# Kernel optimization log

Measured on AMD Instinct MI355X. Metric: run time of the kernel, lower is better.

## Reference

```python
import jax, jax.numpy as jnp
import numpy as np

DIM = 1024
H = 16
DH = 64
INTER = H * DH

def setup_inputs() -> dict:
    key = jax.random.key(0)
    k1, k2, k3, k4 = jax.random.split(key, 4)
    input = jax.random.normal(k1, (4, 2048, DIM), dtype=jnp.float32)
    # nn.Linear weights stored as [out, in]; we keep [in, out] for x @ W
    W_qkv = jax.random.normal(k2, (DIM, INTER * 3), dtype=jnp.float32) * 0.02
    W_mlp = jax.random.normal(k3, (INTER, DIM), dtype=jnp.float32) * 0.02
    b_mlp = jax.random.normal(k4, (DIM,), dtype=jnp.float32) * 0.02
    return {"input": input, "W_qkv": W_qkv, "W_mlp": W_mlp, "b_mlp": b_mlp}

def reference(input, W_qkv, W_mlp, b_mlp):
    b, n, _ = input.shape
    qkv = input @ W_qkv                      # [b, n, 3*h*d]
    qkv = qkv.reshape(b, n, 3, H, DH)        # matches '(qkv h d)' split order
    qkv = jnp.transpose(qkv, (2, 0, 3, 1, 4))  # [3, b, h, n, d]
    q, k, v = qkv[0], qkv[1], qkv[2]
    scale = DH ** -0.5
    attn = jnp.einsum('bhnd,bhmd->bhnm', q, k) * scale
    attn = jax.nn.softmax(attn, axis=-1)
    out = jnp.einsum('bhnm,bhmd->bhnd', attn, v)
    out = jnp.transpose(out, (0, 2, 1, 3)).reshape(b, n, INTER)  # 'b h n d -> b n (h d)'
    return out @ W_mlp + b_mlp
```

## Files before the change

kernel.cpp:

```cpp
#include <hip/hip_runtime.h>
#include <stdint.h>

typedef __attribute__((ext_vector_type(8))) short bf16x8;
typedef __attribute__((ext_vector_type(4))) float f32x4;
typedef __attribute__((ext_vector_type(16))) float f32x16;

#define MFMA16(a, b, c) __builtin_amdgcn_mfma_f32_16x16x32_bf16((a), (b), (c), 0, 0, 0)
#define MFMA32(a, b, c) __builtin_amdgcn_mfma_f32_32x32x16_bf16((a), (b), (c), 0, 0, 0)

__device__ __forceinline__ unsigned short f2bf(float x) {
  uint32_t u = __float_as_uint(x);
  u += 0x7fffu + ((u >> 16) & 1u);
  return (unsigned short)(u >> 16);
}

__device__ __forceinline__ uint32_t cvt_pk_bf16(float a, float b) {
  uint32_t r;
  asm("v_cvt_pk_bf16_f32 %0, %1, %2" : "=v"(r) : "v"(a), "v"(b));
  return r;
}

__device__ __forceinline__ float exp2_hw(float x) {
  float r;
  asm("v_exp_f32 %0, %1" : "=v"(r) : "v"(x));
  return r;
}

__device__ __forceinline__ void gload_lds16(const void* g, void* l) {
  __builtin_amdgcn_global_load_lds(
      (const __attribute__((address_space(1))) uint32_t*)g,
      (__attribute__((address_space(3))) uint32_t*)l, 16, 0, 0);
}

__global__ __launch_bounds__(256) void prep_kernel(
    const float* __restrict__ X, unsigned short* __restrict__ Xb,
    const float* __restrict__ Wq, unsigned short* __restrict__ Wqt,
    const float* __restrict__ Wm, unsigned short* __restrict__ Wmt) {
  __shared__ float tile[64][65];
  const int bid = blockIdx.x;
  const int t = threadIdx.x;
  if (bid < 4096) {
    const int i = bid * 256 + t;
    const float4 a = *(const float4*)(X + (size_t)i * 8);
    const float4 b = *(const float4*)(X + (size_t)i * 8 + 4);
    uint4 o;
    o.x = (uint32_t)f2bf(a.x) | ((uint32_t)f2bf(a.y) << 16);
    o.y = (uint32_t)f2bf(a.z) | ((uint32_t)f2bf(a.w) << 16);
    o.z = (uint32_t)f2bf(b.x) | ((uint32_t)f2bf(b.y) << 16);
    o.w = (uint32_t)f2bf(b.z) | ((uint32_t)f2bf(b.w) << 16);
    *(uint4*)(Xb + (size_t)i * 8) = o;
    return;
  }
  const float* src;
  unsigned short* dst;
  int Nd, lb;
  if (bid < 4864) { src = Wq; dst = Wqt; Nd = 3072; lb = bid - 4096; }
  else            { src = Wm; dst = Wmt; Nd = 1024; lb = bid - 4864; }
  const int Kd = 1024;
  const int ntc = Nd >> 6;
  const int r0 = (lb / ntc) << 6;
  const int c0 = (lb % ntc) << 6;
  const int tr = t >> 4;
  const int tc4 = (t & 15) << 2;
#pragma unroll
  for (int p = 0; p < 4; ++p) {
    int row = p * 16 + tr;
    float4 v = *(const float4*)(src + (size_t)(r0 + row) * Nd + c0 + tc4);
    tile[row][tc4 + 0] = v.x;
    tile[row][tc4 + 1] = v.y;
    tile[row][tc4 + 2] = v.z;
    tile[row][tc4 + 3] = v.w;
  }
  __syncthreads();
#pragma unroll
  for (int p = 0; p < 4; ++p) {
    int c = p * 16 + tr;
    int r4 = (t & 15) << 2;
    uint2 pv;
    pv.x = (uint32_t)f2bf(tile[r4 + 0][c]) | ((uint32_t)f2bf(tile[r4 + 1][c]) << 16);
    pv.y = (uint32_t)f2bf(tile[r4 + 2][c]) | ((uint32_t)f2bf(tile[r4 + 3][c]) << 16);
    *(uint2*)(dst + (size_t)(c0 + c) * Kd + r0 + r4) = pv;
  }
}

__global__ __launch_bounds__(256) void gemm_qkv_kernel(
    const unsigned short* __restrict__ A,
    const unsigned short* __restrict__ Bt,
    unsigned short* __restrict__ Qo,
    unsigned short* __restrict__ Ko,
    unsigned short* __restrict__ Vo) {
  constexpr int Kdim = 1024, BK = 64;
  __shared__ unsigned short lA[128 * BK];
  __shared__ unsigned short lB[128 * BK];
  const int nbn = 24;
  const int wg = (blockIdx.x & 7) * 192 + (blockIdx.x >> 3);
  const int bi = wg / nbn, bj = wg % nbn;
  const int tid = threadIdx.x;
  const int l = tid & 63, w = tid >> 6;
  const int wr = w >> 1, wc = w & 1;
  const int lr = l & 15, lg = l >> 4;

  const f32x4 vzero = {0.f, 0.f, 0.f, 0.f};
  f32x4 acc[4][4];
#pragma unroll
  for (int i = 0; i < 4; ++i)
#pragma unroll
    for (int j = 0; j < 4; ++j) acc[i][j] = vzero;

  const int srow = tid >> 3;
  const int sc = tid & 7;
  const int sg = sc ^ (srow & 7);
  const unsigned short* As = A + (size_t)(bi * 128 + srow) * Kdim + sg * 8;
  const unsigned short* Bs = Bt + (size_t)(bj * 128 + srow) * Kdim + sg * 8;
  unsigned short* dA = &lA[(srow * 8 + sc) * 8];
  unsigned short* dB = &lB[(srow * 8 + sc) * 8];

  for (int kt = 0; kt < Kdim / BK; ++kt) {
    const int k0 = kt * BK;
#pragma unroll
    for (int rr = 0; rr < 4; ++rr) {
      gload_lds16(As + (size_t)rr * 32 * Kdim + k0, dA + rr * 32 * BK);
      gload_lds16(Bs + (size_t)rr * 32 * Kdim + k0, dB + rr * 32 * BK);
    }
    __syncthreads();
#pragma unroll
    for (int kk = 0; kk < 2; ++kk) {
      bf16x8 af[4], bfr[4];
#pragma unroll
      for (int it = 0; it < 4; ++it) {
        int r = wr * 64 + it * 16 + lr;
        af[it] = *(const bf16x8*)&lA[r * BK + (((kk * 4 + lg) ^ (lr & 7)) * 8)];
      }
#pragma unroll
      for (int jt = 0; jt < 4; ++jt) {
        int r = wc * 64 + jt * 16 + lr;
        bfr[jt] = *(const bf16x8*)&lB[r * BK + (((kk * 4 + lg) ^ (lr & 7)) * 8)];
      }
#pragma unroll
      for (int it = 0; it < 4; ++it)
#pragma unroll
        for (int jt = 0; jt < 4; ++jt)
          acc[it][jt] = MFMA16(af[it], bfr[jt], acc[it][jt]);
    }
    __syncthreads();
  }

#pragma unroll
  for (int jt = 0; jt < 4; ++jt) {
    const int col = bj * 128 + wc * 64 + jt * 16 + lr;
    const int s = col >> 10;
    const int rem = col & 1023;
    const int h = rem >> 6, d = rem & 63;
#pragma unroll
    for (int it = 0; it < 4; ++it) {
      const int m0 = bi * 128 + wr * 64 + it * 16 + lg * 4;
      const int b = m0 >> 11, n = m0 & 2047;
      const size_t bh = (size_t)b * 16 + h;
      if (s == 2) {
        uint2 pv;
        pv.x = (uint32_t)f2bf(acc[it][jt][0]) | ((uint32_t)f2bf(acc[it][jt][1]) << 16);
        pv.y = (uint32_t)f2bf(acc[it][jt][2]) | ((uint32_t)f2bf(acc[it][jt][3]) << 16);
        *(uint2*)(Vo + ((bh * 256 + (n >> 3)) * 64 + d) * 8 + (n & 7)) = pv;
      } else if (s == 1) {
        const size_t base = ((bh * 8 + (d >> 3)) * 2048) * 8 + (d & 7);
#pragma unroll
        for (int rg = 0; rg < 4; ++rg)
          Ko[base + (size_t)(n + rg) * 8] = f2bf(acc[it][jt][rg]);
      } else {
#pragma unroll
        for (int rg = 0; rg < 4; ++rg)
          Qo[(bh * 2048 + (size_t)(n + rg)) * 64 + d] = f2bf(acc[it][jt][rg] * 0.18033688011112042f);
      }
    }
  }
}

template <int T>
__device__ __forceinline__ bf16x8 build_pa(const f32x16& s, int hi) {
  uint32_t A1 = cvt_pk_bf16(s[T * 8 + 0], s[T * 8 + 1]);
  uint32_t A2 = cvt_pk_bf16(s[T * 8 + 2], s[T * 8 + 3]);
  uint32_t B1 = cvt_pk_bf16(s[T * 8 + 4], s[T * 8 + 5]);
  uint32_t B2 = cvt_pk_bf16(s[T * 8 + 6], s[T * 8 + 7]);
  uint32_t send1 = hi ? A1 : B1;
  uint32_t send2 = hi ? A2 : B2;
  uint32_t recv1 = (uint32_t)__shfl_xor((int)send1, 32);
  uint32_t recv2 = (uint32_t)__shfl_xor((int)send2, 32);
  union { uint32_t u[4]; bf16x8 v; } r;
  r.u[0] = hi ? recv1 : A1;
  r.u[1] = hi ? recv2 : A2;
  r.u[2] = hi ? B1 : recv1;
  r.u[3] = hi ? B2 : recv2;
  return r.v;
}

__device__ __forceinline__ float tile_sum(const f32x16& a, const f32x16& b) {
  float st[8];
#pragma unroll
  for (int i = 0; i < 8; ++i) st[i] = (a[i] + a[i + 8]) + (b[i] + b[i + 8]);
  float sm = ((st[0] + st[1]) + (st[2] + st[3])) + ((st[4] + st[5]) + (st[6] + st[7]));
  sm += __shfl_xor(sm, 32);
  return sm;
}

#define STAGE(NB, T)                                                              \
  {                                                                               \
    const int kv0_ = (T) * 64;                                                    \
    gload_lds16(KgB + (size_t)(0 * 2048 + kv0_) * 8 + (size_t)(w) * 2048 * 8,     \
                &lK[NB][w][l][0]);                                                \
    gload_lds16(KgB + (size_t)(4 * 2048 + kv0_) * 8 + (size_t)(w) * 2048 * 8,     \
                &lK[NB][w + 4][l][0]);                                            \
    gload_lds16(VgB + (size_t)(((T) * 8 + w) * 64) * 8, &lV[NB][w][l][0]);        \
    gload_lds16(VgB + (size_t)(((T) * 8 + w + 4) * 64) * 8, &lV[NB][w + 4][l][0]);\
  }

__global__ __launch_bounds__(256, 2) void attn_kernel(
    const unsigned short* __restrict__ Qg,
    const unsigned short* __restrict__ Kg,
    const unsigned short* __restrict__ Vg,
    unsigned short* __restrict__ AO) {
  __shared__ unsigned short lK[2][8][64][8];
  __shared__ unsigned short lV[2][8][64][8];
  const int bid = blockIdx.x;
  const int bh = (bid & 7) * 8 + (bid >> 6);
  const int qt = (bid >> 3) & 7;
  const int tid = threadIdx.x;
  const int l = tid & 63, w = tid >> 6;
  const int lo = l & 31, hi = l >> 5;
  const int qb = qt * 256 + w * 64;

  bf16x8 qfA[4], qfB[4];
  {
    const unsigned short* qrowA = Qg + ((size_t)bh * 2048 + qb + lo) * 64 + hi * 8;
    const unsigned short* qrowB = qrowA + 32 * 64;
#pragma unroll
    for (int ds = 0; ds < 4; ++ds) {
      qfA[ds] = *(const bf16x8*)(qrowA + ds * 16);
      qfB[ds] = *(const bf16x8*)(qrowB + ds * 16);
    }
  }

  f32x16 oA0, oA1, oB0, oB1;
#pragma unroll
  for (int i = 0; i < 16; ++i) { oA0[i] = 0.f; oA1[i] = 0.f; oB0[i] = 0.f; oB1[i] = 0.f; }
  float lA_ = 0.f, lB_ = 0.f;

  const unsigned short* KgB = Kg + (size_t)bh * 8 * 2048 * 8 + (size_t)l * 8;
  const unsigned short* VgB = Vg + (size_t)bh * 256 * 64 * 8 + (size_t)l * 8;

  STAGE(0, 0);
  int buf = 0;
  for (int t = 0; t < 32; ++t) {
    if (t < 31) {
      STAGE(buf ^ 1, t + 1);
      asm volatile("s_waitcnt vmcnt(8)" ::: "memory");
    } else {
      asm volatile("s_waitcnt vmcnt(0)" ::: "memory");
    }
    __builtin_amdgcn_s_barrier();
    __builtin_amdgcn_sched_barrier(0);

    f32x16 sA0, sA1, sB0, sB1;
#pragma unroll
    for (int i = 0; i < 16; ++i) { sA0[i] = 0.f; sA1[i] = 0.f; sB0[i] = 0.f; sB1[i] = 0.f; }
    __builtin_amdgcn_s_setprio(1);
#pragma unroll
    for (int ds = 0; ds < 4; ++ds) {
      bf16x8 k0 = *(const bf16x8*)&lK[buf][2 * ds + hi][lo][0];
      bf16x8 k1 = *(const bf16x8*)&lK[buf][2 * ds + hi][lo + 32][0];
      sA0 = MFMA32(k0, qfA[ds], sA0);
      sA1 = MFMA32(k1, qfA[ds], sA1);
      sB0 = MFMA32(k0, qfB[ds], sB0);
      sB1 = MFMA32(k1, qfB[ds], sB1);
    }
    __builtin_amdgcn_s_setprio(0);

#pragma unroll
    for (int i = 0; i < 16; ++i) { sA0[i] = exp2_hw(sA0[i]); sA1[i] = exp2_hw(sA1[i]); }
#pragma unroll
    for (int i = 0; i < 16; ++i) { sB0[i] = exp2_hw(sB0[i]); sB1[i] = exp2_hw(sB1[i]); }
    lA_ += tile_sum(sA0, sA1);
    lB_ += tile_sum(sB0, sB1);

    bf16x8 paA[4] = {build_pa<0>(sA0, hi), build_pa<1>(sA0, hi),
                     build_pa<0>(sA1, hi), build_pa<1>(sA1, hi)};
    bf16x8 paB[4] = {build_pa<0>(sB0, hi), build_pa<1>(sB0, hi),
                     build_pa<0>(sB1, hi), build_pa<1>(sB1, hi)};

    __builtin_amdgcn_s_setprio(1);
#pragma unroll
    for (int ks = 0; ks < 4; ++ks) {
      bf16x8 v0 = *(const bf16x8*)&lV[buf][2 * ks + hi][lo][0];
      bf16x8 v1 = *(const bf16x8*)&lV[buf][2 * ks + hi][lo + 32][0];
      oA0 = MFMA32(v0, paA[ks], oA0);
      oA1 = MFMA32(v1, paA[ks], oA1);
      oB0 = MFMA32(v0, paB[ks], oB0);
      oB1 = MFMA32(v1, paB[ks], oB1);
    }
    __builtin_amdgcn_s_setprio(0);
    __builtin_amdgcn_sched_barrier(0);
    __builtin_amdgcn_s_barrier();
    buf ^= 1;
  }

  const float linvA = 1.0f / lA_;
  const float linvB = 1.0f / lB_;
  const int b = bh >> 4, h = bh & 15;
  unsigned short* dstA = AO + ((size_t)(b * 2048 + qb + lo) * 1024 + h * 64 + 4 * hi);
  unsigned short* dstB = dstA + (size_t)32 * 1024;
#pragma unroll
  for (int q4 = 0; q4 < 4; ++q4) {
    uint2 p0;
    p0.x = cvt_pk_bf16(oA0[q4 * 4 + 0] * linvA, oA0[q4 * 4 + 1] * linvA);
    p0.y = cvt_pk_bf16(oA0[q4 * 4 + 2] * linvA, oA0[q4 * 4 + 3] * linvA);
    *(uint2*)(dstA + q4 * 8) = p0;
    uint2 p1;
    p1.x = cvt_pk_bf16(oA1[q4 * 4 + 0] * linvA, oA1[q4 * 4 + 1] * linvA);
    p1.y = cvt_pk_bf16(oA1[q4 * 4 + 2] * linvA, oA1[q4 * 4 + 3] * linvA);
    *(uint2*)(dstA + 32 + q4 * 8) = p1;
    uint2 p2;
    p2.x = cvt_pk_bf16(oB0[q4 * 4 + 0] * linvB, oB0[q4 * 4 + 1] * linvB);
    p2.y = cvt_pk_bf16(oB0[q4 * 4 + 2] * linvB, oB0[q4 * 4 + 3] * linvB);
    *(uint2*)(dstB + q4 * 8) = p2;
    uint2 p3;
    p3.x = cvt_pk_bf16(oB1[q4 * 4 + 0] * linvB, oB1[q4 * 4 + 1] * linvB);
    p3.y = cvt_pk_bf16(oB1[q4 * 4 + 2] * linvB, oB1[q4 * 4 + 3] * linvB);
    *(uint2*)(dstB + 32 + q4 * 8) = p3;
  }
}

__global__ __launch_bounds__(256) void gemm_mlp_kernel(
    const unsigned short* __restrict__ A,
    const unsigned short* __restrict__ Bt,
    const float* __restrict__ bias,
    float* __restrict__ out) {
  constexpr int Kdim = 1024, BK = 64;
  __shared__ unsigned short lA[128 * BK];
  __shared__ unsigned short lB[128 * BK];
  const int nbn = 8;
  const int wg = (blockIdx.x & 7) * 64 + (blockIdx.x >> 3);
  const int bi = wg / nbn, bj = wg % nbn;
  const int tid = threadIdx.x;
  const int l = tid & 63, w = tid >> 6;
  const int wr = w >> 1, wc = w & 1;
  const int lr = l & 15, lg = l >> 4;

  const f32x4 vzero = {0.f, 0.f, 0.f, 0.f};
  f32x4 acc[4][4];
#pragma unroll
  for (int i = 0; i < 4; ++i)
#pragma unroll
    for (int j = 0; j < 4; ++j) acc[i][j] = vzero;

  const int srow = tid >> 3;
  const int sc = tid & 7;
  const int sg = sc ^ (srow & 7);
  const unsigned short* As = A + (size_t)(bi * 128 + srow) * Kdim + sg * 8;
  const unsigned short* Bs = Bt + (size_t)(bj * 128 + srow) * Kdim + sg * 8;
  unsigned short* dA = &lA[(srow * 8 + sc) * 8];
  unsigned short* dB = &lB[(srow * 8 + sc) * 8];

  for (int kt = 0; kt < Kdim / BK; ++kt) {
    const int k0 = kt * BK;
#pragma unroll
    for (int rr = 0; rr < 4; ++rr) {
      gload_lds16(As + (size_t)rr * 32 * Kdim + k0, dA + rr * 32 * BK);
      gload_lds16(Bs + (size_t)rr * 32 * Kdim + k0, dB + rr * 32 * BK);
    }
    __syncthreads();
#pragma unroll
    for (int kk = 0; kk < 2; ++kk) {
      bf16x8 af[4], bfr[4];
#pragma unroll
      for (int it = 0; it < 4; ++it) {
        int r = wr * 64 + it * 16 + lr;
        af[it] = *(const bf16x8*)&lA[r * BK + (((kk * 4 + lg) ^ (lr & 7)) * 8)];
      }
#pragma unroll
      for (int jt = 0; jt < 4; ++jt) {
        int r = wc * 64 + jt * 16 + lr;
        bfr[jt] = *(const bf16x8*)&lB[r * BK + (((kk * 4 + lg) ^ (lr & 7)) * 8)];
      }
#pragma unroll
      for (int it = 0; it < 4; ++it)
#pragma unroll
        for (int jt = 0; jt < 4; ++jt)
          acc[it][jt] = MFMA16(af[it], bfr[jt], acc[it][jt]);
    }
    __syncthreads();
  }

#pragma unroll
  for (int jt = 0; jt < 4; ++jt) {
    const int col = bj * 128 + wc * 64 + jt * 16 + lr;
    const float bv = bias[col];
#pragma unroll
    for (int it = 0; it < 4; ++it) {
      const int m0 = bi * 128 + wr * 64 + it * 16 + lg * 4;
#pragma unroll
      for (int rg = 0; rg < 4; ++rg)
        out[(size_t)(m0 + rg) * 1024 + col] = acc[it][jt][rg] + bv;
    }
  }
}

extern "C" void kernel_launch(void* const* d_in, const int* in_sizes, int n_in,
                              void* d_out, int out_size, void* d_ws, size_t ws_size,
                              hipStream_t stream) {
  const float* X = (const float*)d_in[0];
  const float* Wqkv = (const float*)d_in[1];
  const float* Wmlp = (const float*)d_in[2];
  const float* bmlp = (const float*)d_in[3];
  float* out = (float*)d_out;

  char* ws = (char*)d_ws;
  unsigned short* Xb  = (unsigned short*)(ws);
  unsigned short* Wqt = (unsigned short*)(ws + 16777216);
  unsigned short* Wmt = (unsigned short*)(ws + 23068672);
  unsigned short* Qb  = (unsigned short*)(ws + 25165824);
  unsigned short* Kb  = (unsigned short*)(ws + 41943040);
  unsigned short* Vb  = (unsigned short*)(ws + 58720256);
  unsigned short* AOb = (unsigned short*)(ws + 75497472);

  prep_kernel<<<5120, 256, 0, stream>>>(X, Xb, Wqkv, Wqt, Wmlp, Wmt);
  gemm_qkv_kernel<<<1536, 256, 0, stream>>>(Xb, Wqt, Qb, Kb, Vb);
  attn_kernel<<<512, 256, 0, stream>>>(Qb, Kb, Vb, AOb);
  gemm_mlp_kernel<<<512, 256, 0, stream>>>(AOb, Wmt, bmlp, out);
}
```

Measured before the change: 192.8 us.

## Load K/V fragments directly from global into registers, dropping LDS staging

Replaces the double-buffered LDS staging of K and V tiles, with its block barriers, by direct per-wave global loads into registers. K for the next tile is prefetched after the QK MFMAs, and V is loaded at the top of each iteration. This removes the LDS traffic and the two barriers per iteration, but each of the four waves now fetches the same K/V data from global/L2 separately. It also raises register pressure and gives less latency hiding for the V loads.

```diff
diff --git a/kernel.cpp b/kernel.cpp
--- a/kernel.cpp
+++ b/kernel.cpp
@@ -202,24 +202,11 @@
   return sm;
 }
 
-#define STAGE(NB, T)                                                              \
-  {                                                                               \
-    const int kv0_ = (T) * 64;                                                    \
-    gload_lds16(KgB + (size_t)(0 * 2048 + kv0_) * 8 + (size_t)(w) * 2048 * 8,     \
-                &lK[NB][w][l][0]);                                                \
-    gload_lds16(KgB + (size_t)(4 * 2048 + kv0_) * 8 + (size_t)(w) * 2048 * 8,     \
-                &lK[NB][w + 4][l][0]);                                            \
-    gload_lds16(VgB + (size_t)(((T) * 8 + w) * 64) * 8, &lV[NB][w][l][0]);        \
-    gload_lds16(VgB + (size_t)(((T) * 8 + w + 4) * 64) * 8, &lV[NB][w + 4][l][0]);\
-  }
-
 __global__ __launch_bounds__(256, 2) void attn_kernel(
     const unsigned short* __restrict__ Qg,
     const unsigned short* __restrict__ Kg,
     const unsigned short* __restrict__ Vg,
     unsigned short* __restrict__ AO) {
-  __shared__ unsigned short lK[2][8][64][8];
-  __shared__ unsigned short lV[2][8][64][8];
   const int bid = blockIdx.x;
   const int bh = (bid & 7) * 8 + (bid >> 6);
   const int qt = (bid >> 3) & 7;
@@ -244,20 +231,22 @@
   for (int i = 0; i < 16; ++i) { oA0[i] = 0.f; oA1[i] = 0.f; oB0[i] = 0.f; oB1[i] = 0.f; }
   float lA_ = 0.f, lB_ = 0.f;
 
-  const unsigned short* KgB = Kg + (size_t)bh * 8 * 2048 * 8 + (size_t)l * 8;
-  const unsigned short* VgB = Vg + (size_t)bh * 256 * 64 * 8 + (size_t)l * 8;
-
-  STAGE(0, 0);
-  int buf = 0;
+  const unsigned short* Kp = Kg + ((size_t)(bh * 8 + hi) * 2048 + lo) * 8;
+  const unsigned short* Vp = Vg + ((size_t)(bh * 256 + hi) * 64 + lo) * 8;
+
+  bf16x8 kf0[4], kf1[4], vf0[4], vf1[4];
+#pragma unroll
+  for (int ds = 0; ds < 4; ++ds) {
+    kf0[ds] = *(const bf16x8*)(Kp + ds * 32768);
+    kf1[ds] = *(const bf16x8*)(Kp + ds * 32768 + 256);
+  }
+
   for (int t = 0; t < 32; ++t) {
-    if (t < 31) {
-      STAGE(buf ^ 1, t + 1);
-      asm volatile("s_waitcnt vmcnt(8)" ::: "memory");
-    } else {
-      asm volatile("s_waitcnt vmcnt(0)" ::: "memory");
-    }
-    __builtin_amdgcn_s_barrier();
-    __builtin_amdgcn_sched_barrier(0);
+#pragma unroll
+    for (int ks = 0; ks < 4; ++ks) {
+      vf0[ks] = *(const bf16x8*)(Vp + (size_t)t * 4096 + ks * 1024);
+      vf1[ks] = *(const bf16x8*)(Vp + (size_t)t * 4096 + ks * 1024 + 256);
+    }
 
     f32x16 sA0, sA1, sB0, sB1;
 #pragma unroll
@@ -265,14 +254,20 @@
     __builtin_amdgcn_s_setprio(1);
 #pragma unroll
     for (int ds = 0; ds < 4; ++ds) {
-      bf16x8 k0 = *(const bf16x8*)&lK[buf][2 * ds + hi][lo][0];
-      bf16x8 k1 = *(const bf16x8*)&lK[buf][2 * ds + hi][lo + 32][0];
-      sA0 = MFMA32(k0, qfA[ds], sA0);
-      sA1 = MFMA32(k1, qfA[ds], sA1);
-      sB0 = MFMA32(k0, qfB[ds], sB0);
-      sB1 = MFMA32(k1, qfB[ds], sB1);
+      sA0 = MFMA32(kf0[ds], qfA[ds], sA0);
+      sA1 = MFMA32(kf1[ds], qfA[ds], sA1);
+      sB0 = MFMA32(kf0[ds], qfB[ds], sB0);
+      sB1 = MFMA32(kf1[ds], qfB[ds], sB1);
     }
     __builtin_amdgcn_s_setprio(0);
+
+    if (t < 31) {
+#pragma unroll
+      for (int ds = 0; ds < 4; ++ds) {
+        kf0[ds] = *(const bf16x8*)(Kp + (size_t)(t + 1) * 512 + ds * 32768);
+        kf1[ds] = *(const bf16x8*)(Kp + (size_t)(t + 1) * 512 + ds * 32768 + 256);
+      }
+    }
 
 #pragma unroll
     for (int i = 0; i < 16; ++i) { sA0[i] = exp2_hw(sA0[i]); sA1[i] = exp2_hw(sA1[i]); }
@@ -289,17 +284,12 @@
     __builtin_amdgcn_s_setprio(1);
 #pragma unroll
     for (int ks = 0; ks < 4; ++ks) {
-      bf16x8 v0 = *(const bf16x8*)&lV[buf][2 * ks + hi][lo][0];
-      bf16x8 v1 = *(const bf16x8*)&lV[buf][2 * ks + hi][lo + 32][0];
-      oA0 = MFMA32(v0, paA[ks], oA0);
-      oA1 = MFMA32(v1, paA[ks], oA1);
-      oB0 = MFMA32(v0, paB[ks], oB0);
-      oB1 = MFMA32(v1, paB[ks], oB1);
+      oA0 = MFMA32(vf0[ks], paA[ks], oA0);
+      oA1 = MFMA32(vf1[ks], paA[ks], oA1);
+      oB0 = MFMA32(vf0[ks], paB[ks], oB0);
+      oB1 = MFMA32(vf1[ks], paB[ks], oB1);
     }
     __builtin_amdgcn_s_setprio(0);
-    __builtin_amdgcn_sched_barrier(0);
-    __builtin_amdgcn_s_barrier();
-    buf ^= 1;
   }
 
   const float linvA = 1.0f / lA_;
```

Measured after the change: 191.5 us. About the same (-0.6%).
